# Kernel optimization log

Measured on AMD Instinct MI355X. Metric: run time of the kernel, lower is better.

## Reference

```python
import jax, jax.numpy as jnp
import numpy as np

C = 256
DQK = C // 8


def setup_inputs() -> dict:
    key = jax.random.key(0)
    ks = jax.random.split(key, 7)
    B, H, W = 8, 64, 64
    x = jax.random.normal(ks[0], (B, H, W, C), dtype=jnp.float32)
    # 1x1 conv weights (equivalent to per-pixel dense): [Cin, Cout] + bias
    sq = 1.0 / np.sqrt(C)
    Wq = jax.random.normal(ks[1], (C, DQK), dtype=jnp.float32) * sq
    bq = jnp.zeros((DQK,), dtype=jnp.float32)
    Wk = jax.random.normal(ks[2], (C, DQK), dtype=jnp.float32) * sq
    bk = jnp.zeros((DQK,), dtype=jnp.float32)
    Wv = jax.random.normal(ks[3], (C, C), dtype=jnp.float32) * sq
    bv = jnp.zeros((C,), dtype=jnp.float32)
    gamma = jnp.float32(0.5)  # nonzero so attention path affects output/grads
    return {"x": x, "Wq": Wq, "bq": bq, "Wk": Wk, "bk": bk,
            "Wv": Wv, "bv": bv, "gamma": gamma}


def reference(x, Wq, bq, Wk, bk, Wv, bv, gamma):
    B, H, W, c = x.shape
    n = H * W
    xf = x.reshape(B, n, c)                      # [B, hw, C]
    q = xf @ Wq + bq                              # [B, hw, C//8]
    k = xf @ Wk + bk                              # [B, hw, C//8]
    v = xf @ Wv + bv                              # [B, hw, C]
    scores = jnp.einsum('bnd,bmd->bnm', q, k)     # [B, hw, hw], no scaling (faithful)
    attn = jax.nn.softmax(scores, axis=-1)
    out = jnp.einsum('bnm,bmc->bnc', attn, v)     # [B, hw, C]
    out = out.reshape(B, H, W, c)
    return gamma * out + x
```

## Files before the change

kernel.cpp:

```cpp
#include <hip/hip_runtime.h>
#include <hip/hip_bf16.h>
#include <math.h>

#define B_ 8
#define N_ 4096
#define C_ 256
#define DQK_ 32

typedef float f32x4  __attribute__((ext_vector_type(4)));
typedef float f32x16 __attribute__((ext_vector_type(16)));
typedef short bf16x8 __attribute__((ext_vector_type(8)));
typedef short bf16x4 __attribute__((ext_vector_type(4)));

__device__ __forceinline__ short f2bf(float f){
  union { float f; unsigned u; } v; v.f = f;
  unsigned r = v.u + 0x7fffu + ((v.u >> 16) & 1u);
  return (short)(r >> 16);
}

__global__ void cast_wt_kernel(const float* __restrict__ Wq, const float* __restrict__ Wk,
                               const float* __restrict__ Wv, short* __restrict__ WT){
  int n = blockIdx.x;
  int k = threadIdx.x;
  float val;
  if (n < 32)       val = Wq[k*32 + n];
  else if (n < 64)  val = Wk[k*32 + (n-32)];
  else              val = Wv[k*256 + (n-64)];
  WT[n*256 + k] = f2bf(val);
}

__global__ __launch_bounds__(256) void proj_kernel(
    const float* __restrict__ x, const short* __restrict__ WT,
    const float* __restrict__ bq, const float* __restrict__ bk, const float* __restrict__ bv,
    short* __restrict__ qws, short* __restrict__ kws, short* __restrict__ vSw){
  __shared__ __align__(16) short sX[64*264];
  __shared__ __align__(16) short sT[64*72];
  int tid = threadIdx.x;
  int lane = tid & 63, wave = tid >> 6;
  int lane15 = lane & 15, quad = lane >> 4;
  int mbase = blockIdx.x * 64;
  int b = mbase >> 12, kvb = mbase & (N_-1);

  const float* xr = x + (size_t)mbase * C_;
  for (int i = 0; i < 8; i++){
    int s = tid + i*256;
    int row = s >> 5, cg = (s & 31) << 3;
    const f32x4* src = (const f32x4*)(xr + row*C_ + cg);
    f32x4 a = src[0], c = src[1];
    bf16x8 p;
    p[0]=f2bf(a[0]); p[1]=f2bf(a[1]); p[2]=f2bf(a[2]); p[3]=f2bf(a[3]);
    p[4]=f2bf(c[0]); p[5]=f2bf(c[1]); p[6]=f2bf(c[2]); p[7]=f2bf(c[3]);
    *(bf16x8*)(sX + row*264 + cg) = p;
  }
  __syncthreads();

  f32x4 acc[5][4];
  for (int i=0;i<5;i++) for (int mt=0;mt<4;mt++) acc[i][mt] = (f32x4)(0.f);

  for (int kc = 0; kc < 8; kc++){
    bf16x8 afr[4];
    #pragma unroll
    for (int mt=0;mt<4;mt++)
      afr[mt] = *(const bf16x8*)(sX + (mt*16+lane15)*264 + kc*32 + quad*8);
    bf16x8 bfr[5];
    #pragma unroll
    for (int i=0;i<5;i++){
      int t = i*4 + wave;
      bfr[i] = *(const bf16x8*)(WT + (size_t)(t*16+lane15)*256 + kc*32 + quad*8);
    }
    #pragma unroll
    for (int i=0;i<5;i++)
      #pragma unroll
      for (int mt=0;mt<4;mt++)
        acc[i][mt] = __builtin_amdgcn_mfma_f32_16x16x32_bf16(afr[mt], bfr[i], acc[i][mt], 0,0,0);
  }

  #pragma unroll
  for (int i=0;i<5;i++){
    int t = i*4 + wave;
    int n0 = t*16 + lane15;
    float bias = (n0 < 32) ? bq[n0] : (n0 < 64 ? bk[n0-32] : bv[n0-64]);
    if (n0 < 64){
      #pragma unroll
      for (int mt=0;mt<4;mt++)
        #pragma unroll
        for (int r=0;r<4;r++)
          sT[(mt*16 + quad*4 + r)*72 + n0] = f2bf(acc[i][mt][r] + bias);
    } else {
      int ch = n0 - 64, cht = ch >> 5, c5 = ch & 31;
      int lanep = c5 | ((quad & 1) << 5);
      int jo = (quad >> 1) * 4;
      #pragma unroll
      for (int mt=0;mt<4;mt++){
        bf16x4 pk;
        pk[0]=f2bf(acc[i][mt][0]+bias); pk[1]=f2bf(acc[i][mt][1]+bias);
        pk[2]=f2bf(acc[i][mt][2]+bias); pk[3]=f2bf(acc[i][mt][3]+bias);
        size_t off = (size_t)b*1048576 + (size_t)(kvb>>6)*16384
                   + (size_t)(mt*8 + cht)*512 + (size_t)lanep*8 + jo;
        *(bf16x4*)(vSw + off) = pk;
      }
    }
  }
  __syncthreads();

  {
    int qt = tid >> 7, p = (tid >> 6) & 1, ln = tid & 63;
    int row = qt*32 + (ln & 31);
    int dcol = p*16 + (ln >> 5)*8;
    bf16x8 vq = *(const bf16x8*)(sT + row*72 + dcol);
    bf16x8 vk = *(const bf16x8*)(sT + row*72 + 32 + dcol);
    size_t qoff = ((((size_t)b*128 + ((kvb>>5) + qt))*2 + p)*64 + ln)*8;
    *(bf16x8*)(qws + qoff) = vq;
    size_t koff = ((size_t)b*64 + (kvb>>6))*2048 + (size_t)((qt*2 + p)*64 + ln)*8;
    *(bf16x8*)(kws + koff) = vk;
  }
}

__global__ __launch_bounds__(512, 2) void flash_kernel(
    const float* __restrict__ x, const short* __restrict__ qws, const short* __restrict__ kws,
    const short* __restrict__ vSw, const float* __restrict__ gptr, float* __restrict__ out){
  __shared__ __align__(16) char smem[67584];
  short* sV0 = (short*)smem;
  short* sV1 = (short*)(smem + 32768);
  int tid = threadIdx.x;
  int lane = tid & 63, wave = tid >> 6;
  int l31 = lane & 31, h = lane >> 5;
  int qp = wave >> 2, cd = (wave >> 1) & 1, kh = wave & 1;
  int b = blockIdx.x & 7;
  int q0 = (blockIdx.x >> 3) << 7;

  const short* qb = qws + (size_t)b*131072;
  const short* kb = kws + (size_t)b*131072;
  const short* vb = vSw + (size_t)b*1048576;

  int qtgA = (q0 >> 5) + qp*2;
  bf16x8 qfA0 = *(const bf16x8*)(qb + (size_t)((qtgA*2+0)*64 + lane)*8);
  bf16x8 qfA1 = *(const bf16x8*)(qb + (size_t)((qtgA*2+1)*64 + lane)*8);
  bf16x8 qfB0 = *(const bf16x8*)(qb + (size_t)(((qtgA+1)*2+0)*64 + lane)*8);
  bf16x8 qfB1 = *(const bf16x8*)(qb + (size_t)(((qtgA+1)*2+1)*64 + lane)*8);

  const short* kf0p = kb + (size_t)((2*kh+0)*64 + lane)*8;
  const short* kf1p = kb + (size_t)((2*kh+1)*64 + lane)*8;
  bf16x8 kfc0 = *(const bf16x8*)(kf0p);
  bf16x8 kfc1 = *(const bf16x8*)(kf1p);

#define VPREF(CHUNK, DST) do { \
    const short* vsrc_ = vb + (size_t)(CHUNK)*16384; \
    _Pragma("unroll") \
    for (int r_=0;r_<4;r_++) \
      __builtin_amdgcn_global_load_lds( \
        (const __attribute__((address_space(1))) void*)(vsrc_ + (size_t)(r_*512+tid)*8), \
        (__attribute__((address_space(3))) void*)((DST) + (size_t)(r_*512+tid)*8), 16, 0, 0); \
  } while(0)

#define EXPPACK(S, PF, RS) do { \
    float ls_ = 0.f; \
    _Pragma("unroll") \
    for (int g_=0; g_<2; g_++){ \
      union { bf16x8 v; unsigned u[4]; } P_; \
      _Pragma("unroll") \
      for (int j_=0;j_<4;j_++){ \
        float2 e_; \
        e_.x = __expf((S)[g_*8 + 2*j_]); \
        e_.y = __expf((S)[g_*8 + 2*j_ + 1]); \
        ls_ += e_.x + e_.y; \
        __hip_bfloat162 t2_ = __float22bfloat162_rn(e_); \
        __builtin_memcpy(&P_.u[j_], &t2_, 4); \
      } \
      (PF)[g_] = P_.v; \
    } \
    (RS) += ls_; \
  } while(0)

  VPREF(0, sV0);
  __syncthreads();

  f32x16 accA[4], accB[4];
  #pragma unroll
  for (int t=0;t<4;t++){ accA[t] = (f32x16)(0.f); accB[t] = (f32x16)(0.f); }
  float rsA = 0.f, rsB = 0.f;

  for (int it=0; it<64; it++){
    short* sVc = (it & 1) ? sV1 : sV0;
    short* sVn = (it & 1) ? sV0 : sV1;
    if (it < 63) VPREF(it+1, sVn);

    bf16x8 pfA[2], pfB[2];
    {
      f32x16 s = __builtin_amdgcn_mfma_f32_32x32x16_bf16(kfc0, qfA0, (f32x16)(0.f), 0,0,0);
      s        = __builtin_amdgcn_mfma_f32_32x32x16_bf16(kfc1, qfA1, s, 0,0,0);
      EXPPACK(s, pfA, rsA);
    }
    {
      f32x16 s = __builtin_amdgcn_mfma_f32_32x32x16_bf16(kfc0, qfB0, (f32x16)(0.f), 0,0,0);
      s        = __builtin_amdgcn_mfma_f32_32x32x16_bf16(kfc1, qfB1, s, 0,0,0);
      EXPPACK(s, pfB, rsB);
    }
    if (it < 63){
      kfc0 = *(const bf16x8*)(kf0p + (size_t)(it+1)*2048);
      kfc1 = *(const bf16x8*)(kf1p + (size_t)(it+1)*2048);
    }

    #pragma unroll
    for (int ks=0; ks<2; ks++){
      const short* base = sVc + (2*kh + ks)*4096;
      #pragma unroll
      for (int c=0; c<4; c++){
        bf16x8 vf = *(const bf16x8*)(base + ((cd*4+c)*64 + lane)*8);
        accA[c] = __builtin_amdgcn_mfma_f32_32x32x16_bf16(pfA[ks], vf, accA[c], 0,0,0);
        accB[c] = __builtin_amdgcn_mfma_f32_32x32x16_bf16(pfB[ks], vf, accB[c], 0,0,0);
      }
    }
    __syncthreads();
  }

  rsA += __shfl_xor(rsA, 32);
  rsB += __shfl_xor(rsB, 32);
  float* R  = (float*)smem;
  float* RS = (float*)(smem + 65536);
  int pw = wave ^ 1;
  if (cd == 0 && lane < 32){ RS[wave*64 + l31] = rsA; RS[wave*64 + 32 + l31] = rsB; }

  if (kh == 0){
    #pragma unroll
    for (int i=0;i<16;i++){ R[wave*2048 + i*64 + lane] = accB[0][i];
                            R[wave*2048 + 1024 + i*64 + lane] = accB[1][i]; }
  } else {
    #pragma unroll
    for (int i=0;i<16;i++){ R[wave*2048 + i*64 + lane] = accA[0][i];
                            R[wave*2048 + 1024 + i*64 + lane] = accA[1][i]; }
  }
  __syncthreads();
  if (kh == 0){
    #pragma unroll
    for (int i=0;i<16;i++){ accA[0][i] += R[pw*2048 + i*64 + lane];
                            accA[1][i] += R[pw*2048 + 1024 + i*64 + lane]; }
  } else {
    #pragma unroll
    for (int i=0;i<16;i++){ accB[0][i] += R[pw*2048 + i*64 + lane];
                            accB[1][i] += R[pw*2048 + 1024 + i*64 + lane]; }
  }
  __syncthreads();
  if (kh == 0){
    #pragma unroll
    for (int i=0;i<16;i++){ R[wave*2048 + i*64 + lane] = accB[2][i];
                            R[wave*2048 + 1024 + i*64 + lane] = accB[3][i]; }
  } else {
    #pragma unroll
    for (int i=0;i<16;i++){ R[wave*2048 + i*64 + lane] = accA[2][i];
                            R[wave*2048 + 1024 + i*64 + lane] = accA[3][i]; }
  }
  __syncthreads();
  if (kh == 0){
    #pragma unroll
    for (int i=0;i<16;i++){ accA[2][i] += R[pw*2048 + i*64 + lane];
                            accA[3][i] += R[pw*2048 + 1024 + i*64 + lane]; }
  } else {
    #pragma unroll
    for (int i=0;i<16;i++){ accB[2][i] += R[pw*2048 + i*64 + lane];
                            accB[3][i] += R[pw*2048 + 1024 + i*64 + lane]; }
  }

  float g = *gptr;
  int kt = qp*2 + kh;
  int w0 = qp*4, w1 = qp*4 + 1;
  int sel = kh*32;
  const float* xb = x + ((size_t)b*N_ + q0 + kt*32)*C_;
  float*       ob = out + ((size_t)b*N_ + q0 + kt*32)*C_;
  if (kh == 0){
    #pragma unroll
    for (int i=0;i<16;i++){
      int q = (i&3) + 8*(i>>2) + 4*h;
      float rv = 1.f / (RS[w0*64 + sel + q] + RS[w1*64 + sel + q]);
      #pragma unroll
      for (int c=0;c<4;c++){
        int ch = (cd*4 + c)*32 + l31;
        ob[(size_t)q*C_ + ch] = g*(accA[c][i]*rv) + xb[(size_t)q*C_ + ch];
      }
    }
  } else {
    #pragma unroll
    for (int i=0;i<16;i++){
      int q = (i&3) + 8*(i>>2) + 4*h;
      float rv = 1.f / (RS[w0*64 + sel + q] + RS[w1*64 + sel + q]);
      #pragma unroll
      for (int c=0;c<4;c++){
        int ch = (cd*4 + c)*32 + l31;
        ob[(size_t)q*C_ + ch] = g*(accB[c][i]*rv) + xb[(size_t)q*C_ + ch];
      }
    }
  }
#undef VPREF
#undef EXPPACK
}

extern "C" void kernel_launch(void* const* d_in, const int* in_sizes, int n_in,
                              void* d_out, int out_size, void* d_ws, size_t ws_size,
                              hipStream_t stream){
  const float* x  = (const float*)d_in[0];
  const float* Wq = (const float*)d_in[1];
  const float* bq = (const float*)d_in[2];
  const float* Wk = (const float*)d_in[3];
  const float* bk = (const float*)d_in[4];
  const float* Wv = (const float*)d_in[5];
  const float* bv = (const float*)d_in[6];
  const float* gm = (const float*)d_in[7];
  float* out = (float*)d_out;
  char* ws = (char*)d_ws;
  short* WT  = (short*)ws;
  short* qws = (short*)(ws + 163840);
  short* kws = (short*)(ws + 163840 + 2097152);
  short* vSw = (short*)(ws + 163840 + 2*2097152);

  cast_wt_kernel<<<dim3(320), dim3(256), 0, stream>>>(Wq, Wk, Wv, WT);
  proj_kernel<<<dim3(512), dim3(256), 0, stream>>>(x, WT, bq, bk, bv, qws, kws, vSw);
  flash_kernel<<<dim3(256), dim3(512), 0, stream>>>(x, qws, kws, vSw, gm, out);
}
```

Before: 197.9 us.

## Split QK/softmax work across wave pairs and exchange P tiles via LDS

Before, both waves of a cd pair each computed scores and exponentials for the same two query tiles. Now each wave computes scores and exp for only one query tile and writes its packed bf16 P fragment to a double-buffered LDS area, where the partner wave (wave^2) reads it. This halves the redundant MFMA and exp work. Score computation is also software-pipelined one iteration ahead of the PV MFMAs. The cost is extra LDS writes and reads each iteration and a rise in shared memory to 96KB, which may limit blocks per CU; with the grid at 256 blocks this likely matters little.

```diff
diff --git a/kernel.cpp b/kernel.cpp
--- a/kernel.cpp
+++ b/kernel.cpp
@@ -119,9 +119,10 @@
 __global__ __launch_bounds__(512, 2) void flash_kernel(
     const float* __restrict__ x, const short* __restrict__ qws, const short* __restrict__ kws,
     const short* __restrict__ vSw, const float* __restrict__ gptr, float* __restrict__ out){
-  __shared__ __align__(16) char smem[67584];
+  __shared__ __align__(16) char smem[98304];
   short* sV0 = (short*)smem;
   short* sV1 = (short*)(smem + 32768);
+  short* pfX = (short*)(smem + 65536);
   int tid = threadIdx.x;
   int lane = tid & 63, wave = tid >> 6;
   int l31 = lane & 31, h = lane >> 5;
@@ -133,11 +134,9 @@
   const short* kb = kws + (size_t)b*131072;
   const short* vb = vSw + (size_t)b*1048576;
 
-  int qtgA = (q0 >> 5) + qp*2;
-  bf16x8 qfA0 = *(const bf16x8*)(qb + (size_t)((qtgA*2+0)*64 + lane)*8);
-  bf16x8 qfA1 = *(const bf16x8*)(qb + (size_t)((qtgA*2+1)*64 + lane)*8);
-  bf16x8 qfB0 = *(const bf16x8*)(qb + (size_t)(((qtgA+1)*2+0)*64 + lane)*8);
-  bf16x8 qfB1 = *(const bf16x8*)(qb + (size_t)(((qtgA+1)*2+1)*64 + lane)*8);
+  int qtg = (q0 >> 5) + qp*2 + cd;
+  bf16x8 qf0 = *(const bf16x8*)(qb + (size_t)((qtg*2+0)*64 + lane)*8);
+  bf16x8 qf1 = *(const bf16x8*)(qb + (size_t)((qtg*2+1)*64 + lane)*8);
 
   const short* kf0p = kb + (size_t)((2*kh+0)*64 + lane)*8;
   const short* kf1p = kb + (size_t)((2*kh+1)*64 + lane)*8;
@@ -153,7 +152,7 @@
         (__attribute__((address_space(3))) void*)((DST) + (size_t)(r_*512+tid)*8), 16, 0, 0); \
   } while(0)
 
-#define EXPPACK(S, PF, RS) do { \
+#define EXPPACK(S, PF) do { \
     float ls_ = 0.f; \
     _Pragma("unroll") \
     for (int g_=0; g_<2; g_++){ \
@@ -169,57 +168,75 @@
       } \
       (PF)[g_] = P_.v; \
     } \
-    (RS) += ls_; \
+    rsO += ls_; \
   } while(0)
 
+#define PVX(SVC, PA, PB) do { \
+    _Pragma("unroll") \
+    for (int ks_=0; ks_<2; ks_++){ \
+      const short* base_ = (SVC) + (2*kh + ks_)*4096; \
+      _Pragma("unroll") \
+      for (int c_=0; c_<4; c_++){ \
+        bf16x8 vf_ = *(const bf16x8*)(base_ + ((cd*4+c_)*64 + lane)*8); \
+        accA[c_] = __builtin_amdgcn_mfma_f32_32x32x16_bf16((PA)[ks_], vf_, accA[c_], 0,0,0); \
+        accB[c_] = __builtin_amdgcn_mfma_f32_32x32x16_bf16((PB)[ks_], vf_, accB[c_], 0,0,0); \
+      } \
+    } \
+  } while(0)
+
   VPREF(0, sV0);
-  __syncthreads();
 
   f32x16 accA[4], accB[4];
   #pragma unroll
   for (int t=0;t<4;t++){ accA[t] = (f32x16)(0.f); accB[t] = (f32x16)(0.f); }
-  float rsA = 0.f, rsB = 0.f;
+  float rsO = 0.f;
+  bf16x8 pfO[2];
+
+  {
+    f32x16 s = __builtin_amdgcn_mfma_f32_32x32x16_bf16(kfc0, qf0, (f32x16)(0.f), 0,0,0);
+    s        = __builtin_amdgcn_mfma_f32_32x32x16_bf16(kfc1, qf1, s, 0,0,0);
+    EXPPACK(s, pfO);
+    *(bf16x8*)(pfX + ((0*8 + wave)*2 + 0)*512 + lane*8) = pfO[0];
+    *(bf16x8*)(pfX + ((0*8 + wave)*2 + 1)*512 + lane*8) = pfO[1];
+  }
+  kfc0 = *(const bf16x8*)(kf0p + 2048);
+  kfc1 = *(const bf16x8*)(kf1p + 2048);
+  __syncthreads();
 
   for (int it=0; it<64; it++){
     short* sVc = (it & 1) ? sV1 : sV0;
     short* sVn = (it & 1) ? sV0 : sV1;
     if (it < 63) VPREF(it+1, sVn);
 
-    bf16x8 pfA[2], pfB[2];
-    {
-      f32x16 s = __builtin_amdgcn_mfma_f32_32x32x16_bf16(kfc0, qfA0, (f32x16)(0.f), 0,0,0);
-      s        = __builtin_amdgcn_mfma_f32_32x32x16_bf16(kfc1, qfA1, s, 0,0,0);
-      EXPPACK(s, pfA, rsA);
-    }
-    {
-      f32x16 s = __builtin_amdgcn_mfma_f32_32x32x16_bf16(kfc0, qfB0, (f32x16)(0.f), 0,0,0);
-      s        = __builtin_amdgcn_mfma_f32_32x32x16_bf16(kfc1, qfB1, s, 0,0,0);
-      EXPPACK(s, pfB, rsB);
-    }
+    bf16x8 pfN[2];
     if (it < 63){
-      kfc0 = *(const bf16x8*)(kf0p + (size_t)(it+1)*2048);
-      kfc1 = *(const bf16x8*)(kf1p + (size_t)(it+1)*2048);
-    }
-
-    #pragma unroll
-    for (int ks=0; ks<2; ks++){
-      const short* base = sVc + (2*kh + ks)*4096;
-      #pragma unroll
-      for (int c=0; c<4; c++){
-        bf16x8 vf = *(const bf16x8*)(base + ((cd*4+c)*64 + lane)*8);
-        accA[c] = __builtin_amdgcn_mfma_f32_32x32x16_bf16(pfA[ks], vf, accA[c], 0,0,0);
-        accB[c] = __builtin_amdgcn_mfma_f32_32x32x16_bf16(pfB[ks], vf, accB[c], 0,0,0);
-      }
-    }
+      f32x16 s = __builtin_amdgcn_mfma_f32_32x32x16_bf16(kfc0, qf0, (f32x16)(0.f), 0,0,0);
+      s        = __builtin_amdgcn_mfma_f32_32x32x16_bf16(kfc1, qf1, s, 0,0,0);
+      EXPPACK(s, pfN);
+      *(bf16x8*)(pfX + ((((it+1)&1)*8 + wave)*2 + 0)*512 + lane*8) = pfN[0];
+      *(bf16x8*)(pfX + ((((it+1)&1)*8 + wave)*2 + 1)*512 + lane*8) = pfN[1];
+    }
+    if (it < 62){
+      kfc0 = *(const bf16x8*)(kf0p + (size_t)(it+2)*2048);
+      kfc1 = *(const bf16x8*)(kf1p + (size_t)(it+2)*2048);
+    }
+
+    bf16x8 pfP[2];
+    pfP[0] = *(const bf16x8*)(pfX + (((it&1)*8 + (wave^2))*2 + 0)*512 + lane*8);
+    pfP[1] = *(const bf16x8*)(pfX + (((it&1)*8 + (wave^2))*2 + 1)*512 + lane*8);
+
+    if (cd == 0){ PVX(sVc, pfO, pfP); }
+    else        { PVX(sVc, pfP, pfO); }
+
+    if (it < 63){ pfO[0] = pfN[0]; pfO[1] = pfN[1]; }
     __syncthreads();
   }
 
-  rsA += __shfl_xor(rsA, 32);
-  rsB += __shfl_xor(rsB, 32);
+  rsO += __shfl_xor(rsO, 32);
   float* R  = (float*)smem;
   float* RS = (float*)(smem + 65536);
   int pw = wave ^ 1;
-  if (cd == 0 && lane < 32){ RS[wave*64 + l31] = rsA; RS[wave*64 + 32 + l31] = rsB; }
+  if (lane < 32) RS[wave*32 + l31] = rsO;
 
   if (kh == 0){
     #pragma unroll
@@ -263,15 +280,14 @@
 
   float g = *gptr;
   int kt = qp*2 + kh;
-  int w0 = qp*4, w1 = qp*4 + 1;
-  int sel = kh*32;
+  int w0 = qp*4 + kh*2, w1 = w0 + 1;
   const float* xb = x + ((size_t)b*N_ + q0 + kt*32)*C_;
   float*       ob = out + ((size_t)b*N_ + q0 + kt*32)*C_;
   if (kh == 0){
     #pragma unroll
     for (int i=0;i<16;i++){
       int q = (i&3) + 8*(i>>2) + 4*h;
-      float rv = 1.f / (RS[w0*64 + sel + q] + RS[w1*64 + sel + q]);
+      float rv = 1.f / (RS[w0*32 + q] + RS[w1*32 + q]);
       #pragma unroll
       for (int c=0;c<4;c++){
         int ch = (cd*4 + c)*32 + l31;
@@ -282,7 +298,7 @@
     #pragma unroll
     for (int i=0;i<16;i++){
       int q = (i&3) + 8*(i>>2) + 4*h;
-      float rv = 1.f / (RS[w0*64 + sel + q] + RS[w1*64 + sel + q]);
+      float rv = 1.f / (RS[w0*32 + q] + RS[w1*32 + q]);
       #pragma unroll
       for (int c=0;c<4;c++){
         int ch = (cd*4 + c)*32 + l31;
@@ -292,6 +308,7 @@
   }
 #undef VPREF
 #undef EXPPACK
+#undef PVX
 }
 
 extern "C" void kernel_launch(void* const* d_in, const int* in_sizes, int n_in,
```

New measurement: 238.1 us. 1.2x slower.
